# Kernel optimization log

Measured on AMD Instinct MI355X. Metric: run time of the kernel, lower is better.

Reference implementation:

```python
import jax, jax.numpy as jnp
import numpy as np

N_NODES = 100000
N_EDGES = 640000
H = 128

def setup_inputs() -> dict:
    key = jax.random.key(0)
    k = jax.random.split(key, 8)
    x_src = jax.random.normal(k[0], (N_NODES, H), dtype=jnp.float32)
    x_dst = jax.random.normal(k[1], (N_NODES, H), dtype=jnp.float32)
    src_idx = jax.random.randint(k[2], (N_EDGES,), 0, N_NODES, dtype=jnp.int64)
    dst_idx = jax.random.randint(k[3], (N_EDGES,), 0, N_NODES, dtype=jnp.int64)
    # torch Linear default init: U(-1/sqrt(fan_in), 1/sqrt(fan_in)); randn*scale is fine for a numeric baseline
    W1 = jax.random.normal(k[4], (H, 2 * H), dtype=jnp.float32) * (1.0 / np.sqrt(2 * H))
    b1 = jnp.zeros((H,), dtype=jnp.float32)
    W2 = jax.random.normal(k[5], (1, H), dtype=jnp.float32) * (1.0 / np.sqrt(H))
    b2 = jnp.zeros((1,), dtype=jnp.float32)
    return {"x_src": x_src, "x_dst": x_dst, "src_idx": src_idx, "dst_idx": dst_idx,
            "W1": W1, "b1": b1, "W2": W2, "b2": b2}

def reference(x_src, x_dst, src_idx, dst_idx, W1, b1, W2, b2):
    # per-edge gather of endpoint features, concat -> [E, 2H]
    h = jnp.concatenate([x_src[src_idx], x_dst[dst_idx]], axis=1)
    h = jax.nn.relu(h @ W1.T + b1)            # [E, H]
    score = (h @ W2.T + b2)[:, 0]             # [E]
    return score
```

## Files before the change

### kernel.cpp

```cpp
#include <hip/hip_runtime.h>
#include <hip/hip_bf16.h>

typedef __bf16 bf16x8 __attribute__((ext_vector_type(8)));
typedef __bf16 bf16x4 __attribute__((ext_vector_type(4)));
typedef float  f32x4  __attribute__((ext_vector_type(4)));

#define HF 128
#define W1K 256

__global__ __launch_bounds__(256) void w1_repack(
    const float* __restrict__ W1, __bf16* __restrict__ wf)
{
    const int h    = blockIdx.x;
    const int tid  = threadIdx.x;
    const int lane = tid & 63;
    const int wid  = tid >> 6;
    const int l15  = lane & 15;
    const int lg   = lane >> 4;

    for (int f = wid; f < 32; f += 4) {
        const int mt = f >> 2;
        const int kk = f & 3;
        const float* p = W1 + h * HF + (size_t)(mt * 16 + l15) * W1K
                       + kk * 32 + lg * 8;
        f32x4 a = *reinterpret_cast<const f32x4*>(p);
        f32x4 b = *reinterpret_cast<const f32x4*>(p + 4);
        bf16x8 w8;
        #pragma unroll
        for (int i = 0; i < 4; ++i) {
            w8[i]     = (__bf16)a[i];
            w8[i + 4] = (__bf16)b[i];
        }
        *reinterpret_cast<bf16x8*>(wf + ((size_t)(h * 32 + f) * 64 + lane) * 8) = w8;
    }
}

__global__ __launch_bounds__(256, 1) void node_precompute10(
    const float* __restrict__ x_src, const float* __restrict__ x_dst,
    const __bf16* __restrict__ wf,
    __bf16* __restrict__ u, __bf16* __restrict__ v, int nNodes)
{
    __shared__ __align__(16) __bf16 wlds[2][32][64][8];
    __shared__ __align__(16) float  xlds[2][64 * HF];

    const int tid  = threadIdx.x;
    const int lane = tid & 63;
    const int wid  = tid >> 6;
    const int l15  = lane & 15;
    const int lg   = lane >> 4;

    {
        __bf16* wl = &wlds[0][0][0][0];
        for (int c = tid; c < 4096; c += 256) {
            bf16x8 w8 = *reinterpret_cast<const bf16x8*>(wf + (size_t)c * 8);
            *reinterpret_cast<bf16x8*>(wl + (size_t)c * 8) = w8;
        }
    }

    const int nth = (nNodes + 63) >> 6;
    const int T   = nth * 2;

    auto STAGE = [&](int buf, int t) {
        const int h    = t & 1;
        const int trow = t >> 1;
        const float* __restrict__ xp = h ? x_dst : x_src;
        #pragma unroll
        for (int i = 0; i < 8; ++i) {
            const int G   = i * 256 + tid;
            const int row = G >> 5;
            const int q   = G & 31;
            const int qs  = q ^ (row & 7);
            const int grow = min(trow * 64 + row, nNodes - 1);
            const float* src = xp + (size_t)grow * HF + qs * 4;
            __builtin_amdgcn_global_load_lds(
                (const __attribute__((address_space(1))) void*)src,
                (__attribute__((address_space(3))) void*)&xlds[buf][(size_t)G * 4],
                16, 0, 0);
        }
    };

    int t = blockIdx.x;
    if (t >= T) return;
    STAGE(0, t);
    __syncthreads();

    int buf = 0;
    while (t < T) {
        const int tn = t + gridDim.x;
        if (tn < T) STAGE(buf ^ 1, tn);

        const int h    = t & 1;
        const int trow = t >> 1;
        const int row  = wid * 16 + l15;
        const int node = trow * 64 + row;

        f32x4 acc[8];
        #pragma unroll
        for (int mt = 0; mt < 8; ++mt) acc[mt] = (f32x4){0.f, 0.f, 0.f, 0.f};

        const float* xr = &xlds[buf][(size_t)row * HF];
        #pragma unroll
        for (int kk = 0; kk < 4; ++kk) {
            const int q0 = kk * 8 + lg * 2;
            f32x4 a0 = *reinterpret_cast<const f32x4*>(xr + ((q0)     ^ (row & 7)) * 4);
            f32x4 a1 = *reinterpret_cast<const f32x4*>(xr + ((q0 + 1) ^ (row & 7)) * 4);
            bf16x8 xb;
            #pragma unroll
            for (int i = 0; i < 4; ++i) {
                xb[i]     = (__bf16)a0[i];
                xb[i + 4] = (__bf16)a1[i];
            }
            #pragma unroll
            for (int mt = 0; mt < 8; ++mt) {
                bf16x8 wa = *reinterpret_cast<const bf16x8*>(&wlds[h][mt * 4 + kk][lane][0]);
                acc[mt] = __builtin_amdgcn_mfma_f32_16x16x32_bf16(
                    wa, xb, acc[mt], 0, 0, 0);
            }
        }

        if (node < nNodes) {
            __bf16* op = (h ? v : u) + (size_t)node * HF + lg * 4;
            #pragma unroll
            for (int mt = 0; mt < 8; ++mt) {
                bf16x4 o4;
                #pragma unroll
                for (int r = 0; r < 4; ++r) o4[r] = (__bf16)acc[mt][r];
                *reinterpret_cast<bf16x4*>(op + mt * 16) = o4;
            }
        }

        __syncthreads();
        buf ^= 1;
        t = tn;
    }
}

__global__ __launch_bounds__(256) void edge_score_kernel(
    const __bf16* __restrict__ u, const __bf16* __restrict__ v,
    const int* __restrict__ sidx, const int* __restrict__ didx,
    const float* __restrict__ W2, const float* __restrict__ b1,
    const float* __restrict__ b2,
    float* __restrict__ out, int nEdges)
{
    const int tid = threadIdx.x;
    const int sub = tid >> 4;
    const int l16 = tid & 15;

    const int ebase = blockIdx.x * 64 + sub;

    float w2v[8], b1v[8];
    #pragma unroll
    for (int j = 0; j < 8; ++j) {
        w2v[j] = W2[l16 * 8 + j];
        b1v[j] = b1[l16 * 8 + j];
    }
    const float b2v = b2[0];

    int e[4], si[4], di[4];
    #pragma unroll
    for (int q = 0; q < 4; ++q) {
        e[q] = ebase + q * 16;
        const int c = min(e[q], nEdges - 1);
        si[q] = sidx[c];
        di[q] = didx[c];
    }

    bf16x8 uv[4], vv[4];
    #pragma unroll
    for (int q = 0; q < 4; ++q) {
        uv[q] = *reinterpret_cast<const bf16x8*>(u + (size_t)si[q] * HF + l16 * 8);
        vv[q] = *reinterpret_cast<const bf16x8*>(v + (size_t)di[q] * HF + l16 * 8);
    }

    float s[4] = {0.f, 0.f, 0.f, 0.f};
    #pragma unroll
    for (int q = 0; q < 4; ++q)
        #pragma unroll
        for (int j = 0; j < 8; ++j)
            s[q] += fmaxf((float)uv[q][j] + (float)vv[q][j] + b1v[j], 0.f) * w2v[j];

    #pragma unroll
    for (int off = 1; off < 16; off <<= 1)
        #pragma unroll
        for (int q = 0; q < 4; ++q)
            s[q] += __shfl_xor(s[q], off, 64);

    if (l16 == 0) {
        #pragma unroll
        for (int q = 0; q < 4; ++q)
            if (e[q] < nEdges) out[e[q]] = s[q] + b2v;
    }
}

__global__ __launch_bounds__(256, 2) void edge_mlp_kernel(
    const float* __restrict__ x_src, const float* __restrict__ x_dst,
    const int*   __restrict__ src_idx, const int* __restrict__ dst_idx,
    const float* __restrict__ W1, const float* __restrict__ b1,
    const float* __restrict__ W2, const float* __restrict__ b2,
    float* __restrict__ out, int nEdges)
{
    __shared__ __align__(16) __bf16 w1lds[64 * 64 * 8];

    const int tid  = threadIdx.x;
    const int lane = tid & 63;
    const int wid  = tid >> 6;
    const int l15  = lane & 15;
    const int lg   = lane >> 4;

    for (int p = wid; p < 64; p += 4) {
        const int n   = p >> 3;
        const int kk  = p & 7;
        const float* src = W1 + (n * 16 + l15) * W1K + kk * 32 + lg * 8;
        bf16x8 w8;
        #pragma unroll
        for (int i = 0; i < 8; ++i) w8[i] = (__bf16)src[i];
        *reinterpret_cast<bf16x8*>(&w1lds[(p * 64 + lane) * 8]) = w8;
    }
    __syncthreads();

    float w2v[8], b1v[8];
    #pragma unroll
    for (int n = 0; n < 8; ++n) {
        w2v[n] = W2[n * 16 + l15];
        b1v[n] = b1[n * 16 + l15];
    }
    const float b2v = b2[0];

    const int ntiles = nEdges / 256;
    for (int t = blockIdx.x; t < ntiles; t += gridDim.x) {
        const int ebase = t * 256 + wid * 64;

        const float* srow[4];
        const float* drow[4];
        #pragma unroll
        for (int m = 0; m < 4; ++m) {
            const int e  = ebase + m * 16 + l15;
            srow[m] = x_src + (size_t)src_idx[e] * HF + lg * 8;
            drow[m] = x_dst + (size_t)dst_idx[e] * HF + lg * 8;
        }

        f32x4 acc[4][8];
        #pragma unroll
        for (int m = 0; m < 4; ++m)
            #pragma unroll
            for (int n = 0; n < 8; ++n)
                acc[m][n] = (f32x4){0.f, 0.f, 0.f, 0.f};

        #pragma unroll
        for (int kk = 0; kk < 8; ++kk) {
            bf16x8 a[4];
            #pragma unroll
            for (int m = 0; m < 4; ++m) {
                const float* p = (kk < 4) ? (srow[m] + kk * 32)
                                          : (drow[m] + (kk - 4) * 32);
                f32x4 u0 = *reinterpret_cast<const f32x4*>(p);
                f32x4 u1 = *reinterpret_cast<const f32x4*>(p + 4);
                bf16x8 av;
                #pragma unroll
                for (int i = 0; i < 4; ++i) {
                    av[i]     = (__bf16)u0[i];
                    av[i + 4] = (__bf16)u1[i];
                }
                a[m] = av;
            }
            #pragma unroll
            for (int n = 0; n < 8; ++n) {
                bf16x8 bfrag = *reinterpret_cast<const bf16x8*>(
                    &w1lds[((n * 8 + kk) * 64 + lane) * 8]);
                #pragma unroll
                for (int m = 0; m < 4; ++m) {
                    acc[m][n] = __builtin_amdgcn_mfma_f32_16x16x32_bf16(
                        a[m], bfrag, acc[m][n], 0, 0, 0);
                }
            }
        }

        #pragma unroll
        for (int m = 0; m < 4; ++m) {
            float part[4];
            #pragma unroll
            for (int r = 0; r < 4; ++r) {
                float s = 0.f;
                #pragma unroll
                for (int n = 0; n < 8; ++n) {
                    float hv = acc[m][n][r] + b1v[n];
                    s += fmaxf(hv, 0.f) * w2v[n];
                }
                part[r] = s;
            }
            #pragma unroll
            for (int off = 1; off < 16; off <<= 1) {
                #pragma unroll
                for (int r = 0; r < 4; ++r)
                    part[r] += __shfl_xor(part[r], off, 64);
            }
            if (l15 == m) {
                f32x4 v4 = { part[0] + b2v, part[1] + b2v,
                             part[2] + b2v, part[3] + b2v };
                *reinterpret_cast<f32x4*>(&out[ebase + m * 16 + lg * 4]) = v4;
            }
        }
    }
}

extern "C" void kernel_launch(void* const* d_in, const int* in_sizes, int n_in,
                              void* d_out, int out_size, void* d_ws, size_t ws_size,
                              hipStream_t stream) {
    const float* x_src  = (const float*)d_in[0];
    const float* x_dst  = (const float*)d_in[1];
    const int*   sidx   = (const int*)d_in[2];
    const int*   didx   = (const int*)d_in[3];
    const float* W1     = (const float*)d_in[4];
    const float* b1     = (const float*)d_in[5];
    const float* W2     = (const float*)d_in[6];
    const float* b2     = (const float*)d_in[7];
    float* out = (float*)d_out;

    const int nEdges = in_sizes[2];
    const int nNodes = in_sizes[0] / HF;

    const size_t uvsz   = (size_t)2 * nNodes * HF;
    const size_t needed = uvsz * sizeof(__bf16) + 64 * 1024;
    if (ws_size >= needed) {
        __bf16* u  = (__bf16*)d_ws;
        __bf16* v  = u + (size_t)nNodes * HF;
        __bf16* wf = u + uvsz;

        w1_repack<<<2, 256, 0, stream>>>(W1, wf);

        node_precompute10<<<256, 256, 0, stream>>>(
            x_src, x_dst, wf, u, v, nNodes);

        const int egrid = (nEdges + 63) / 64;
        edge_score_kernel<<<egrid, 256, 0, stream>>>(
            u, v, sidx, didx, W2, b1, b2, out, nEdges);
    } else {
        edge_mlp_kernel<<<512, 256, 0, stream>>>(
            x_src, x_dst, sidx, didx, W1, b1, W2, b2, out, nEdges);
    }
}
```

Baseline: 87.64 us.

## Give each wave its own 8-node tile pipeline without block barriers

The node precompute kernel now runs 512 threads per block. Each wave independently stages 8-node tiles into a private double-buffered LDS region and waits on them with s_waitcnt vmcnt instead of block-wide __syncthreads. This removes cross-wave barrier stalls and lets each wave overlap its own loads with compute. In exchange, each 16-row MFMA tile now holds only 8 valid rows, so half of the MFMA work and lane outputs are wasted, and correctness relies on the hand-set vmcnt count being right.

```diff
diff --git a/kernel.cpp b/kernel.cpp
--- a/kernel.cpp
+++ b/kernel.cpp
@@ -35,13 +35,13 @@
     }
 }
 
-__global__ __launch_bounds__(256, 1) void node_precompute10(
+__global__ __launch_bounds__(512, 1) void node_precompute12(
     const float* __restrict__ x_src, const float* __restrict__ x_dst,
     const __bf16* __restrict__ wf,
     __bf16* __restrict__ u, __bf16* __restrict__ v, int nNodes)
 {
     __shared__ __align__(16) __bf16 wlds[2][32][64][8];
-    __shared__ __align__(16) float  xlds[2][64 * HF];
+    __shared__ __align__(16) float  xlds[8][2][1024];
 
     const int tid  = threadIdx.x;
     const int lane = tid & 63;
@@ -51,59 +51,62 @@
 
     {
         __bf16* wl = &wlds[0][0][0][0];
-        for (int c = tid; c < 4096; c += 256) {
+        for (int c = tid; c < 4096; c += 512) {
             bf16x8 w8 = *reinterpret_cast<const bf16x8*>(wf + (size_t)c * 8);
             *reinterpret_cast<bf16x8*>(wl + (size_t)c * 8) = w8;
         }
     }
-
-    const int nth = (nNodes + 63) >> 6;
-    const int T   = nth * 2;
+    __syncthreads();
+
+    const int nst = (nNodes + 7) >> 3;
+    const int T   = nst * 2;
+    const int stride = gridDim.x * 8;
 
     auto STAGE = [&](int buf, int t) {
         const int h    = t & 1;
         const int trow = t >> 1;
         const float* __restrict__ xp = h ? x_dst : x_src;
         #pragma unroll
-        for (int i = 0; i < 8; ++i) {
-            const int G   = i * 256 + tid;
+        for (int i = 0; i < 4; ++i) {
+            const int G   = i * 64 + lane;
             const int row = G >> 5;
             const int q   = G & 31;
-            const int qs  = q ^ (row & 7);
-            const int grow = min(trow * 64 + row, nNodes - 1);
+            const int qs  = q ^ row;
+            const int grow = min(trow * 8 + row, nNodes - 1);
             const float* src = xp + (size_t)grow * HF + qs * 4;
             __builtin_amdgcn_global_load_lds(
                 (const __attribute__((address_space(1))) void*)src,
-                (__attribute__((address_space(3))) void*)&xlds[buf][(size_t)G * 4],
+                (__attribute__((address_space(3))) void*)&xlds[wid][buf][(size_t)G * 4],
                 16, 0, 0);
         }
     };
 
-    int t = blockIdx.x;
+    int t = (blockIdx.x * 8 + wid);
     if (t >= T) return;
     STAGE(0, t);
-    __syncthreads();
 
     int buf = 0;
+    const int row_l = l15 & 7;
     while (t < T) {
-        const int tn = t + gridDim.x;
+        const int tn = t + stride;
         if (tn < T) STAGE(buf ^ 1, tn);
+
+        asm volatile("s_waitcnt vmcnt(12)" ::: "memory");
+        __builtin_amdgcn_sched_barrier(0);
 
         const int h    = t & 1;
         const int trow = t >> 1;
-        const int row  = wid * 16 + l15;
-        const int node = trow * 64 + row;
 
         f32x4 acc[8];
         #pragma unroll
         for (int mt = 0; mt < 8; ++mt) acc[mt] = (f32x4){0.f, 0.f, 0.f, 0.f};
 
-        const float* xr = &xlds[buf][(size_t)row * HF];
+        const float* xr = &xlds[wid][buf][(size_t)row_l * 128];
         #pragma unroll
         for (int kk = 0; kk < 4; ++kk) {
             const int q0 = kk * 8 + lg * 2;
-            f32x4 a0 = *reinterpret_cast<const f32x4*>(xr + ((q0)     ^ (row & 7)) * 4);
-            f32x4 a1 = *reinterpret_cast<const f32x4*>(xr + ((q0 + 1) ^ (row & 7)) * 4);
+            f32x4 a0 = *reinterpret_cast<const f32x4*>(xr + ((q0)     ^ row_l) * 4);
+            f32x4 a1 = *reinterpret_cast<const f32x4*>(xr + ((q0 + 1) ^ row_l) * 4);
             bf16x8 xb;
             #pragma unroll
             for (int i = 0; i < 4; ++i) {
@@ -118,7 +121,8 @@
             }
         }
 
-        if (node < nNodes) {
+        const int node = trow * 8 + l15;
+        if (l15 < 8 && node < nNodes) {
             __bf16* op = (h ? v : u) + (size_t)node * HF + lg * 4;
             #pragma unroll
             for (int mt = 0; mt < 8; ++mt) {
@@ -129,7 +133,6 @@
             }
         }
 
-        __syncthreads();
         buf ^= 1;
         t = tn;
     }
@@ -328,7 +331,7 @@
 
         w1_repack<<<2, 256, 0, stream>>>(W1, wf);
 
-        node_precompute10<<<256, 256, 0, stream>>>(
+        node_precompute12<<<256, 512, 0, stream>>>(
             x_src, x_dst, wf, u, v, nNodes);
 
         const int egrid = (nEdges + 63) / 64;
```

Measured after the change: 83.87 us. 4.3% less time.
